# Kernel tuning notes

Hardware: AMD Instinct MI355X
Metric: run time of the kernel (lower is better)

## Reference

```python
import jax, jax.numpy as jnp
import numpy as np

B, S, E = 2, 2048, 2048
HQ, HKV, D = 16, 4, 128
WINDOW = 512
ROPE_BASE = 10000.0


def apply_rope(x):
    # x: [B, H, S, D]; rotate-half RoPE, positions start at 0 (prefill, no cache)
    half = x.shape[-1] // 2
    inv_freq = 1.0 / (ROPE_BASE ** (jnp.arange(half, dtype=jnp.float32) / half))
    ang = jnp.arange(x.shape[2], dtype=jnp.float32)[:, None] * inv_freq[None, :]  # [S, half]
    cos, sin = jnp.cos(ang), jnp.sin(ang)
    x1, x2 = x[..., :half], x[..., half:]
    return jnp.concatenate([x1 * cos - x2 * sin, x1 * sin + x2 * cos], axis=-1)


def setup_inputs() -> dict:
    key = jax.random.key(0)
    ks = jax.random.split(key, 9)
    sc = 0.02
    return {
        "x": jax.random.normal(ks[0], (B, S, E), dtype=jnp.float32),
        "Wq": jax.random.normal(ks[1], (HQ * D, E), dtype=jnp.float32) * sc,
        "bq": jnp.zeros((HQ * D,), dtype=jnp.float32),
        "Wk": jax.random.normal(ks[2], (HKV * D, E), dtype=jnp.float32) * sc,
        "bk": jnp.zeros((HKV * D,), dtype=jnp.float32),
        "Wv": jax.random.normal(ks[3], (HKV * D, E), dtype=jnp.float32) * sc,
        "bv": jnp.zeros((HKV * D,), dtype=jnp.float32),
        "Wo": jax.random.normal(ks[4], (E, HQ * D), dtype=jnp.float32) * sc,
        "bo": jnp.zeros((E,), dtype=jnp.float32),
    }


def reference(x, Wq, bq, Wk, bk, Wv, bv, Wo, bo):
    b, s, _ = x.shape
    group = HQ // HKV
    # projections (torch Linear: y = x @ W.T + b)
    Q = (x @ Wq.T + bq).reshape(b, s, HQ, D).transpose(0, 2, 1, 3)     # [B,HQ,S,D]
    K = (x @ Wk.T + bk).reshape(b, s, HKV, D).transpose(0, 2, 1, 3)    # [B,HKV,S,D]
    V = (x @ Wv.T + bv).reshape(b, s, HKV, D).transpose(0, 2, 1, 3)
    Q = apply_rope(Q)
    K = apply_rope(K)
    # GQA: group query heads per KV head instead of repeating K/V (same math)
    Qg = Q.reshape(b, HKV, group, s, D)
    scores = jnp.einsum('bkgqd,bkyd->bkgqy', Qg, K) / jnp.sqrt(jnp.float32(D))
    # sliding-window causal mask: j <= i and i - j <= window_size
    i = jnp.arange(s)[:, None]
    j = jnp.arange(s)[None, :]
    allowed = (j <= i) & ((i - j) <= WINDOW)
    scores = jnp.where(allowed, scores, jnp.float32(-jnp.inf))
    w = jax.nn.softmax(scores, axis=-1)
    out = jnp.einsum('bkgqy,bkyd->bkgqd', w, V)                        # [B,HKV,G,S,D]
    out = out.reshape(b, HQ, s, D).transpose(0, 2, 1, 3).reshape(b, s, HQ * D)
    out = out @ Wo.T + bo  # dropout is identity at inference
    return out
```

## Files before the change

### kernel.cpp

```cpp
#include <hip/hip_runtime.h>
#include <hip/hip_bf16.h>

typedef unsigned short u16;
typedef unsigned int u32;
typedef __attribute__((ext_vector_type(4))) unsigned short ushort4_t;
typedef __attribute__((ext_vector_type(8))) short short8;
typedef __attribute__((ext_vector_type(4))) float f32x4;

#define B_ 2
#define S_ 2048
#define E_ 2048
#define HQ_ 16
#define HKV_ 4
#define D_ 128
#define WINDOW_ 512

static __device__ __forceinline__ float bf2f(u16 u) {
    union { unsigned int i; float f; } v; v.i = ((unsigned int)u) << 16; return v.f;
}
static __device__ __forceinline__ u16 f2bf(float f) {
    unsigned int x = __float_as_uint(f);
    unsigned int r = (x + 0x7fffu + ((x >> 16) & 1u)) >> 16;
    return (u16)r;
}

static __device__ __forceinline__ void gload_lds16(const u16* g, u16* l) {
    __builtin_amdgcn_global_load_lds(
        (const __attribute__((address_space(1))) unsigned int*)g,
        (__attribute__((address_space(3))) unsigned int*)l,
        16, 0, 0);
}

static __device__ __forceinline__ int detect_fp32(const u16* wq, int* cnt_sh) {
    if (threadIdx.x == 0) *cnt_sh = 0;
    __syncthreads();
    int c = 0;
    #pragma unroll
    for (int k = 0; k < 4; ++k) {
        u16 v = wq[threadIdx.x * 4 + k];
        if (((v >> 7) & 0xFF) >= 0x90) c++;
    }
    atomicAdd(cnt_sh, c);
    __syncthreads();
    return (*cnt_sh >= 64) ? 1 : 0;
}

#define C_WQ   8388608u
#define C_WK   12582912u
#define C_WV   13631488u
#define C_BQ   14680064u
#define C_BK   14682112u
#define C_BV   14682624u
#define C_WO   14683136u
#define C_BO   18877440u
#define NTOT   18879488u

__global__ __launch_bounds__(256) void convert_kernel(
    const void* p0, const void* p1, const void* p2, const void* p3, const void* p4,
    const void* p5, const void* p6, const void* p7, const void* p8,
    u16* __restrict__ C, int* __restrict__ flagout)
{
    __shared__ int cnt;
    const int f = detect_fp32((const u16*)p1, &cnt);
    if (blockIdx.x == 0 && threadIdx.x == 0) *flagout = f;

    unsigned int idx = (blockIdx.x * 256u + threadIdx.x) * 4u;
    if (idx >= NTOT) return;

    const void* src; unsigned int local;
    if      (idx < C_WQ) { src = p0; local = idx; }
    else if (idx < C_WK) { src = p1; local = idx - C_WQ; }
    else if (idx < C_WV) { src = p3; local = idx - C_WK; }
    else if (idx < C_BQ) { src = p5; local = idx - C_WV; }
    else if (idx < C_BK) { src = p2; local = idx - C_BQ; }
    else if (idx < C_BV) { src = p4; local = idx - C_BK; }
    else if (idx < C_WO) { src = p6; local = idx - C_BV; }
    else if (idx < C_BO) { src = p7; local = idx - C_WO; }
    else                 { src = p8; local = idx - C_BO; }

    ushort4_t o;
    if (f) {
        float4 v = *(const float4*)((const float*)src + local);
        o[0] = f2bf(v.x); o[1] = f2bf(v.y); o[2] = f2bf(v.z); o[3] = f2bf(v.w);
    } else {
        o = *(const ushort4_t*)((const u16*)src + local);
    }
    *(ushort4_t*)(C + idx) = o;
}

__global__ __launch_bounds__(512, 2) void gemm256(
    const u16* __restrict__ A, const u16* __restrict__ W,
    const u16* __restrict__ bias, u16* __restrict__ C,
    int M, int N, int K)
{
    __shared__ __align__(16) u16 lds[65536];

    const int m0 = blockIdx.y * 256, n0 = blockIdx.x * 256;
    const int t = threadIdx.x;
    const int wv = t >> 6, lane = t & 63;
    const int wm = wv >> 2, wn = wv & 3;
    const int quad = lane >> 4, l16 = lane & 15;
    const int h3 = l16 & 7;

    const int rr = t >> 3;
    const int sblk = ((t & 7) ^ (rr & 7)) * 8;

    const u16* Asrc = A + (size_t)(m0 + rr) * K + sblk;
    const u16* Bsrc = W + (size_t)(n0 + rr) * K + sblk;
    u16* ldsA = lds + wv * 512;
    u16* ldsB = lds + 16384 + wv * 512;

#define STAGE_A(slot, Qi, k0) gload_lds16(Asrc + (size_t)((Qi) * 64) * K + (k0), ldsA + (slot) * 32768 + (Qi) * 4096)
#define STAGE_B(slot, Qi, k0) gload_lds16(Bsrc + (size_t)((Qi) * 64) * K + (k0), ldsB + (slot) * 32768 + (Qi) * 4096)

    f32x4 acc[8][4];
    #pragma unroll
    for (int mi = 0; mi < 8; ++mi)
        #pragma unroll
        for (int ni = 0; ni < 4; ++ni)
            acc[mi][ni] = (f32x4){0.f, 0.f, 0.f, 0.f};

    const int NT = K / 64;

    #pragma unroll
    for (int q = 0; q < 4; ++q) STAGE_A(0, q, 0);
    #pragma unroll
    for (int q = 0; q < 4; ++q) STAGE_B(0, q, 0);
    __builtin_amdgcn_sched_barrier(0);
    #pragma unroll
    for (int q = 0; q < 4; ++q) STAGE_A(1, q, 64);
    #pragma unroll
    for (int q = 0; q < 4; ++q) STAGE_B(1, q, 64);
    __builtin_amdgcn_sched_barrier(0);

    short8 afr[4][2];
    short8 b0[2][2], b1[2][2];

#define DSREAD_A(qm_)                                                          \
    _Pragma("unroll")                                                          \
    for (int f = 0; f < 4; ++f) {                                              \
        const int r = wm * 128 + (qm_) * 64 + f * 16 + l16;                    \
        _Pragma("unroll")                                                      \
        for (int kk = 0; kk < 2; ++kk)                                         \
            afr[f][kk] = *(const short8*)(As + r * 64 + (((kk * 4 + quad) ^ h3) << 3)); \
    }

#define DSREAD_B(dst, qn_)                                                     \
    _Pragma("unroll")                                                          \
    for (int g = 0; g < 2; ++g) {                                              \
        const int r = wn * 64 + (qn_) * 32 + g * 16 + l16;                     \
        _Pragma("unroll")                                                      \
        for (int kk = 0; kk < 2; ++kk)                                         \
            dst[g][kk] = *(const short8*)(Bs + r * 64 + (((kk * 4 + quad) ^ h3) << 3)); \
    }

#define SYNC_MFMA(qm_, bsel, qn_)                                              \
    __builtin_amdgcn_sched_barrier(0);                                         \
    __builtin_amdgcn_s_barrier();                                              \
    asm volatile("s_waitcnt lgkmcnt(0)" ::: "memory");                         \
    __builtin_amdgcn_sched_barrier(0);                                         \
    __builtin_amdgcn_s_setprio(1);                                             \
    _Pragma("unroll")                                                          \
    for (int g = 0; g < 2; ++g)                                                \
        _Pragma("unroll")                                                      \
        for (int f = 0; f < 4; ++f)                                            \
            _Pragma("unroll")                                                  \
            for (int kk = 0; kk < 2; ++kk)                                     \
                acc[(qm_) * 4 + f][(qn_) * 2 + g] =                            \
                    __builtin_amdgcn_mfma_f32_16x16x32_bf16(                   \
                        afr[f][kk], bsel[g][kk], acc[(qm_) * 4 + f][(qn_) * 2 + g], 0, 0, 0); \
    __builtin_amdgcn_s_setprio(0);                                             \
    __builtin_amdgcn_sched_barrier(0);                                         \
    __builtin_amdgcn_s_barrier();                                              \
    __builtin_amdgcn_sched_barrier(0);

    for (int kt = 0; kt < NT; ++kt) {
        const int slot = kt & 1;
        const u16* As = lds + slot * 32768;
        const u16* Bs = As + 16384;

        if (kt == 0)           asm volatile("s_waitcnt vmcnt(8)" ::: "memory");
        else if (kt == NT - 1) asm volatile("s_waitcnt vmcnt(0)" ::: "memory");
        else                   asm volatile("s_waitcnt vmcnt(2)" ::: "memory");
        __builtin_amdgcn_s_barrier();
        __builtin_amdgcn_sched_barrier(0);

        const int kB = (kt + 1) * 64;
        const int kA = (kt + 2) * 64;
        const int sB = slot ^ 1;
        const bool doB = (kt >= 1) && (kt <= NT - 2);
        const bool doA = (kt <= NT - 3);

        DSREAD_A(0);
        DSREAD_B(b0, 0);
        if (doB) { STAGE_A(sB, 1, kB); STAGE_A(sB, 3, kB);
                   STAGE_B(sB, 0, kB); STAGE_B(sB, 1, kB); }
        SYNC_MFMA(0, b0, 0);

        DSREAD_B(b1, 1);
        if (doB) { STAGE_B(sB, 2, kB); STAGE_B(sB, 3, kB); }
        SYNC_MFMA(0, b1, 1);

        DSREAD_A(1);
        if (doA) { STAGE_A(slot, 0, kA); }
        SYNC_MFMA(1, b1, 1);

        if (doA) { STAGE_A(slot, 2, kA); }
        SYNC_MFMA(1, b0, 0);
    }

#undef STAGE_A
#undef STAGE_B
#undef DSREAD_A
#undef DSREAD_B
#undef SYNC_MFMA

    #pragma unroll
    for (int mi = 0; mi < 8; ++mi) {
        #pragma unroll
        for (int ni = 0; ni < 4; ++ni) {
            const int row0 = m0 + wm * 128 + mi * 16 + quad * 4;
            const int col  = n0 + wn * 64 + ni * 16 + l16;
            const float bb = bf2f(bias[col]);
            #pragma unroll
            for (int r = 0; r < 4; ++r)
                C[(size_t)(row0 + r) * N + col] = f2bf(acc[mi][ni][r] + bb);
        }
    }
}

#define TBK 32

__global__ __launch_bounds__(256) void gemm128_out(
    const u16* __restrict__ A, const u16* __restrict__ W,
    const u16* __restrict__ bias, void* __restrict__ Cout,
    int M, int N, int K, const int* __restrict__ flagp)
{
    __shared__ __align__(16) u16 As[128 * TBK];
    __shared__ __align__(16) u16 Bs[128 * TBK];

    const int m0 = blockIdx.y * 128, n0 = blockIdx.x * 128;

    const int t = threadIdx.x;
    const int wv = t >> 6, lane = t & 63;
    const int waveM = wv >> 1, waveN = wv & 1;
    const int quad = lane >> 4, l16 = lane & 15;

    const int lrow = lane >> 2;
    const int lcol = (lane & 3) * 8;

    f32x4 acc[4][4];
    #pragma unroll
    for (int mi = 0; mi < 4; ++mi)
        #pragma unroll
        for (int ni = 0; ni < 4; ++ni)
            acc[mi][ni] = (f32x4){0.f, 0.f, 0.f, 0.f};

    const u16* ga = A + (size_t)(m0 + wv * 32 + lrow) * K + lcol;
    const u16* gb = W + (size_t)(n0 + wv * 32 + lrow) * K + lcol;
    u16* la0 = As + (wv * 32) * TBK;
    u16* la1 = As + (wv * 32 + 16) * TBK;
    u16* lb0 = Bs + (wv * 32) * TBK;
    u16* lb1 = Bs + (wv * 32 + 16) * TBK;

    for (int k0 = 0; k0 < K; k0 += TBK) {
        __syncthreads();
        gload_lds16(ga + k0, la0);
        gload_lds16(ga + k0 + (size_t)16 * K, la1);
        gload_lds16(gb + k0, lb0);
        gload_lds16(gb + k0 + (size_t)16 * K, lb1);
        __syncthreads();

        short8 af[4];
        #pragma unroll
        for (int mi = 0; mi < 4; ++mi)
            af[mi] = *(const short8*)(As + (waveM * 64 + mi * 16 + l16) * TBK + quad * 8);
        #pragma unroll
        for (int ni = 0; ni < 4; ++ni) {
            short8 bf = *(const short8*)(Bs + (waveN * 64 + ni * 16 + l16) * TBK + quad * 8);
            #pragma unroll
            for (int mi = 0; mi < 4; ++mi)
                acc[mi][ni] = __builtin_amdgcn_mfma_f32_16x16x32_bf16(af[mi], bf, acc[mi][ni], 0, 0, 0);
        }
    }

    const int f = *flagp;
    #pragma unroll
    for (int mi = 0; mi < 4; ++mi) {
        #pragma unroll
        for (int ni = 0; ni < 4; ++ni) {
            int row0 = m0 + waveM * 64 + mi * 16 + quad * 4;
            int col  = n0 + waveN * 64 + ni * 16 + l16;
            float bb = bf2f(bias[col]);
            #pragma unroll
            for (int r = 0; r < 4; ++r) {
                float val = acc[mi][ni][r] + bb;
                size_t idx = (size_t)(row0 + r) * N + col;
                if (f) ((float*)Cout)[idx] = val;
                else   ((u16*)Cout)[idx]   = f2bf(val);
            }
        }
    }
}

#define ROPE_BLOCKS 20480

__global__ __launch_bounds__(256) void rope_transpose(
    u16* __restrict__ QKV, u16* __restrict__ VT)
{
    if (blockIdx.x < ROPE_BLOCKS) {
        const size_t qtot = (size_t)B_ * S_ * HQ_ * 64;
        size_t idx = (size_t)blockIdx.x * 256 + threadIdx.x;

        int d; size_t tok; u16* p;
        if (idx < qtot) {
            d = (int)(idx & 63);
            size_t th = idx >> 6;
            int h = (int)(th & 15);
            tok = th >> 4;
            p = QKV + tok * 3072 + h * 128 + d;
        } else {
            size_t r = idx - qtot;
            d = (int)(r & 63);
            size_t th = r >> 6;
            int kh = (int)(th & 3);
            tok = th >> 2;
            p = QKV + tok * 3072 + 2048 + kh * 128 + d;
        }
        int s = (int)(tok & (S_ - 1));

        float x1 = bf2f(p[0]);
        float x2 = bf2f(p[64]);
        float inv_freq = __expf(-0.14391156514f * (float)d);
        float ang = (float)s * inv_freq;
        float sn, cs;
        __sincosf(ang, &sn, &cs);
        p[0]  = f2bf(x1 * cs - x2 * sn);
        p[64] = f2bf(x1 * sn + x2 * cs);
    } else {
        const int bid = blockIdx.x - ROPE_BLOCKS;
        const int t = threadIdx.x;
        const int s_blk = bid & 63;
        const int dh = (bid >> 6) & 1;
        const int bkh = bid >> 7;
        const int b = bkh >> 2, kh = bkh & 3;

        const int d = dh * 64 + (t & 63);
        const int s0 = s_blk * 32 + (t >> 6) * 8;

        const u16* src = QKV + (size_t)(b * S_ + s0) * 3072 + 2560 + kh * 128 + d;
        short8 v;
        #pragma unroll
        for (int j = 0; j < 8; ++j)
            v[j] = (short)src[(size_t)j * 3072];
        *(short8*)(VT + ((size_t)(bkh * 128 + d)) * S_ + s0) = v;
    }
}

__global__ __launch_bounds__(256) void attn_mfma(
    const u16* __restrict__ QKV, const u16* __restrict__ VT, u16* __restrict__ O)
{
    __shared__ __align__(16) u16 Ks[32 * 136];
    __shared__ __align__(16) u16 Vs[128 * 40];
    __shared__ __align__(16) u16 ps[4][16 * 40];

    const int t = threadIdx.x;
    const int wv = t >> 6, lane = t & 63;
    const int quad = lane >> 4, l16 = lane & 15;

    const int h = blockIdx.x & 15;
    const int tile = (blockIdx.x >> 4) & 31;
    const int b = blockIdx.x >> 9;
    const int kh = h >> 2;

    const int i0b = tile * 64;
    const int i0w = i0b + wv * 16;
    const float scale = 0.08838834764831845f;
    const float CEXP = 8.0f;

    short8 qf[4];
    {
        const u16* qrow = QKV + (size_t)(b * S_ + i0w + l16) * 3072 + h * 128 + quad * 8;
        #pragma unroll
        for (int kc = 0; kc < 4; ++kc)
            qf[kc] = *(const short8*)(qrow + kc * 32);
    }

    short8 ones;
    #pragma unroll
    for (int j = 0; j < 8; ++j) ones[j] = (short)0x3F80;

    f32x4 oc[8];
    #pragma unroll
    for (int c = 0; c < 8; ++c) oc[c] = (f32x4){0.f, 0.f, 0.f, 0.f};
    f32x4 ocl = (f32x4){0.f, 0.f, 0.f, 0.f};

    int jlo = i0b - WINDOW_; if (jlo < 0) jlo = 0;
    const int nblk = (i0b + 64 - jlo) >> 5;

    const u16* VTb = VT + (size_t)(b * 4 + kh) * 128 * S_;

    for (int blk = 0; blk < nblk; ++blk) {
        const int jbase = jlo + blk * 32;
        __syncthreads();
        #pragma unroll
        for (int it = 0; it < 2; ++it) {
            int idx = it * 256 + t;
            int key = idx >> 4;
            int c8  = (idx & 15) * 8;
            int row = ((key & 1) << 4) | (key >> 1);
            short8 kvv = *(const short8*)(QKV + (size_t)(b * S_ + jbase + key) * 3072 + 2048 + kh * 128 + c8);
            *(short8*)(Ks + row * 136 + c8) = kvv;
        }
        #pragma unroll
        for (int it = 0; it < 2; ++it) {
            int idx = it * 256 + t;
            int d = idx >> 2;
            int q4 = idx & 3;
            short8 vvv = *(const short8*)(VTb + (size_t)d * S_ + jbase + q4 * 8);
            *(short8*)(Vs + d * 40 + q4 * 8) = vvv;
        }
        __syncthreads();

        bool active = (jbase <= i0w + 15) && (jbase + 31 >= i0w - WINDOW_);
        if (!active) continue;

        f32x4 sc0 = {0.f,0.f,0.f,0.f}, sc1 = {0.f,0.f,0.f,0.f};
        #pragma unroll
        for (int kc = 0; kc < 4; ++kc) {
            short8 kb0 = *(const short8*)(Ks + l16 * 136 + kc * 32 + quad * 8);
            short8 kb1 = *(const short8*)(Ks + (16 + l16) * 136 + kc * 32 + quad * 8);
            sc0 = __builtin_amdgcn_mfma_f32_16x16x32_bf16(qf[kc], kb0, sc0, 0, 0, 0);
            sc1 = __builtin_amdgcn_mfma_f32_16x16x32_bf16(qf[kc], kb1, sc1, 0, 0, 0);
        }

        const int j0 = jbase + 2 * l16;
        const int iq = i0w + quad * 4;
        u16* pw = ps[wv];
        #pragma unroll
        for (int r = 0; r < 4; ++r) {
            int i = iq + r;
            bool ok0 = (unsigned)(i - j0)     <= (unsigned)WINDOW_;
            bool ok1 = (unsigned)(i - j0 - 1) <= (unsigned)WINDOW_;
            float p0 = ok0 ? __expf(sc0[r] * scale - CEXP) : 0.f;
            float p1 = ok1 ? __expf(sc1[r] * scale - CEXP) : 0.f;
            u32 pk = ((u32)f2bf(p1) << 16) | (u32)f2bf(p0);
            *(u32*)(pw + (quad * 4 + r) * 40 + 2 * l16) = pk;
        }
        short8 pa = *(const short8*)(pw + l16 * 40 + quad * 8);

        #pragma unroll
        for (int c = 0; c < 8; ++c) {
            short8 vb = *(const short8*)(Vs + (c * 16 + l16) * 40 + quad * 8);
            oc[c] = __builtin_amdgcn_mfma_f32_16x16x32_bf16(pa, vb, oc[c], 0, 0, 0);
        }
        ocl = __builtin_amdgcn_mfma_f32_16x16x32_bf16(pa, ones, ocl, 0, 0, 0);
    }

    float inv0[4];
    #pragma unroll
    for (int r = 0; r < 4; ++r) inv0[r] = 1.0f / ocl[r];
    #pragma unroll
    for (int c = 0; c < 8; ++c) {
        #pragma unroll
        for (int r = 0; r < 4; ++r) {
            O[((size_t)(b * S_ + i0w + quad * 4 + r) * HQ_ + h) * D_ + c * 16 + l16] =
                f2bf(oc[c][r] * inv0[r]);
        }
    }
}

extern "C" void kernel_launch(void* const* d_in, const int* in_sizes, int n_in,
                              void* d_out, int out_size, void* d_ws, size_t ws_size,
                              hipStream_t stream)
{
    char* ws = (char*)d_ws;
    u16* Cc   = (u16*)ws;
    int* flag = (int*)(ws + 37758976);
    u16* QKV  = (u16*)(ws + 37759232);
    u16* Ab   = (u16*)(ws + 37759232 + 25165824);

    const u16* xb    = Cc;
    u16*       VT    = Cc;
    const u16* Wqkv  = Cc + C_WQ;
    const u16* bqkv  = Cc + C_BQ;
    const u16* Wob   = Cc + C_WO;
    const u16* bob   = Cc + C_BO;

    const int M = B_ * S_;
    dim3 blk(256);

    convert_kernel<<<dim3(NTOT / 4 / 256), blk, 0, stream>>>(
        d_in[0], d_in[1], d_in[2], d_in[3], d_in[4], d_in[5], d_in[6], d_in[7], d_in[8],
        Cc, flag);

    gemm256<<<dim3(3072 / 256, M / 256), dim3(512), 0, stream>>>(
        xb, Wqkv, bqkv, QKV, M, 3072, E_);

    rope_transpose<<<dim3(ROPE_BLOCKS + 1024), blk, 0, stream>>>(QKV, VT);

    attn_mfma<<<dim3(B_ * HQ_ * (S_ / 64)), blk, 0, stream>>>(QKV, VT, Ab);

    gemm128_out<<<dim3(E_ / 128, M / 128), blk, 0, stream>>>(Ab, Wob, bob, d_out, M, E_, HQ_ * D_, flag);
}
```

Before: 317.4 us.

## Restructure GEMM main loop to one mid-iteration barrier with double A fragments

Rewrites the software pipeline of the projection GEMM inner loop. Both A-fragment halves are now loaded into separate register sets up front, and fine-grained lgkmcnt waits let MFMAs start while later LDS reads are still in flight. The four barrier-bracketed MFMA phases become a single mid-iteration barrier, and the prologue/staging schedule is reshuffled so all B and odd-A quarters are issued together. This cuts synchronisation stalls per k-step at the cost of extra VGPRs for the second A fragment set, which may affect occupancy, and depends on the hand-counted waitcnt values being correct.

Result: no change. 313.6 us (-1.2%).

```diff
diff --git a/kernel.cpp b/kernel.cpp
--- a/kernel.cpp
+++ b/kernel.cpp
@@ -127,22 +127,20 @@
     #pragma unroll
     for (int q = 0; q < 4; ++q) STAGE_B(0, q, 0);
     __builtin_amdgcn_sched_barrier(0);
-    #pragma unroll
-    for (int q = 0; q < 4; ++q) STAGE_A(1, q, 64);
-    #pragma unroll
-    for (int q = 0; q < 4; ++q) STAGE_B(1, q, 64);
+    STAGE_A(1, 0, 64);
+    STAGE_A(1, 2, 64);
     __builtin_amdgcn_sched_barrier(0);
 
-    short8 afr[4][2];
+    short8 aA[4][2], aB[4][2];
     short8 b0[2][2], b1[2][2];
 
-#define DSREAD_A(qm_)                                                          \
+#define DSREAD_A(dst, qm_)                                                     \
     _Pragma("unroll")                                                          \
-    for (int f = 0; f < 4; ++f) {                                              \
-        const int r = wm * 128 + (qm_) * 64 + f * 16 + l16;                    \
+    for (int fr = 0; fr < 4; ++fr) {                                           \
+        const int r = wm * 128 + (qm_) * 64 + fr * 16 + l16;                   \
         _Pragma("unroll")                                                      \
         for (int kk = 0; kk < 2; ++kk)                                         \
-            afr[f][kk] = *(const short8*)(As + r * 64 + (((kk * 4 + quad) ^ h3) << 3)); \
+            dst[fr][kk] = *(const short8*)(As + r * 64 + (((kk * 4 + quad) ^ h3) << 3)); \
     }
 
 #define DSREAD_B(dst, qn_)                                                     \
@@ -154,66 +152,76 @@
             dst[g][kk] = *(const short8*)(Bs + r * 64 + (((kk * 4 + quad) ^ h3) << 3)); \
     }
 
-#define SYNC_MFMA(qm_, bsel, qn_)                                              \
-    __builtin_amdgcn_sched_barrier(0);                                         \
-    __builtin_amdgcn_s_barrier();                                              \
-    asm volatile("s_waitcnt lgkmcnt(0)" ::: "memory");                         \
-    __builtin_amdgcn_sched_barrier(0);                                         \
+#define MFMA_PH(qm_, afrag, bfrag, qn_)                                        \
     __builtin_amdgcn_s_setprio(1);                                             \
     _Pragma("unroll")                                                          \
     for (int g = 0; g < 2; ++g)                                                \
         _Pragma("unroll")                                                      \
-        for (int f = 0; f < 4; ++f)                                            \
+        for (int fr = 0; fr < 4; ++fr)                                         \
             _Pragma("unroll")                                                  \
             for (int kk = 0; kk < 2; ++kk)                                     \
-                acc[(qm_) * 4 + f][(qn_) * 2 + g] =                            \
+                acc[(qm_) * 4 + fr][(qn_) * 2 + g] =                           \
                     __builtin_amdgcn_mfma_f32_16x16x32_bf16(                   \
-                        afr[f][kk], bsel[g][kk], acc[(qm_) * 4 + f][(qn_) * 2 + g], 0, 0, 0); \
-    __builtin_amdgcn_s_setprio(0);                                             \
-    __builtin_amdgcn_sched_barrier(0);                                         \
-    __builtin_amdgcn_s_barrier();                                              \
-    __builtin_amdgcn_sched_barrier(0);
+                        afrag[fr][kk], bfrag[g][kk], acc[(qm_) * 4 + fr][(qn_) * 2 + g], 0, 0, 0); \
+    __builtin_amdgcn_s_setprio(0);
 
     for (int kt = 0; kt < NT; ++kt) {
         const int slot = kt & 1;
         const u16* As = lds + slot * 32768;
         const u16* Bs = As + 16384;
 
-        if (kt == 0)           asm volatile("s_waitcnt vmcnt(8)" ::: "memory");
-        else if (kt == NT - 1) asm volatile("s_waitcnt vmcnt(0)" ::: "memory");
-        else                   asm volatile("s_waitcnt vmcnt(2)" ::: "memory");
+        if (kt == NT - 1) asm volatile("s_waitcnt vmcnt(0)" ::: "memory");
+        else              asm volatile("s_waitcnt vmcnt(2)" ::: "memory");
         __builtin_amdgcn_s_barrier();
         __builtin_amdgcn_sched_barrier(0);
 
         const int kB = (kt + 1) * 64;
         const int kA = (kt + 2) * 64;
         const int sB = slot ^ 1;
-        const bool doB = (kt >= 1) && (kt <= NT - 2);
-        const bool doA = (kt <= NT - 3);
-
-        DSREAD_A(0);
+        const bool doEarly = (kt <= NT - 2);
+        const bool doMid   = (kt <= NT - 3);
+
+        DSREAD_A(aA, 0);
         DSREAD_B(b0, 0);
-        if (doB) { STAGE_A(sB, 1, kB); STAGE_A(sB, 3, kB);
-                   STAGE_B(sB, 0, kB); STAGE_B(sB, 1, kB); }
-        SYNC_MFMA(0, b0, 0);
-
+        __builtin_amdgcn_sched_barrier(0);
         DSREAD_B(b1, 1);
-        if (doB) { STAGE_B(sB, 2, kB); STAGE_B(sB, 3, kB); }
-        SYNC_MFMA(0, b1, 1);
-
-        DSREAD_A(1);
-        if (doA) { STAGE_A(slot, 0, kA); }
-        SYNC_MFMA(1, b1, 1);
-
-        if (doA) { STAGE_A(slot, 2, kA); }
-        SYNC_MFMA(1, b0, 0);
+        __builtin_amdgcn_sched_barrier(0);
+
+        if (doEarly) { STAGE_A(sB, 1, kB); STAGE_A(sB, 3, kB);
+                       STAGE_B(sB, 0, kB); STAGE_B(sB, 1, kB);
+                       STAGE_B(sB, 2, kB); STAGE_B(sB, 3, kB); }
+        __builtin_amdgcn_sched_barrier(0);
+
+        asm volatile("s_waitcnt lgkmcnt(4)" ::: "memory");
+        __builtin_amdgcn_sched_barrier(0);
+        DSREAD_A(aB, 1);
+        __builtin_amdgcn_sched_barrier(0);
+
+        MFMA_PH(0, aA, b0, 0);
+        __builtin_amdgcn_sched_barrier(0);
+        asm volatile("s_waitcnt lgkmcnt(8)" ::: "memory");
+        __builtin_amdgcn_sched_barrier(0);
+        MFMA_PH(0, aA, b1, 1);
+        __builtin_amdgcn_sched_barrier(0);
+        asm volatile("s_waitcnt lgkmcnt(0)" ::: "memory");
+        __builtin_amdgcn_sched_barrier(0);
+        __builtin_amdgcn_s_barrier();
+        __builtin_amdgcn_sched_barrier(0);
+
+        if (doMid) { STAGE_A(slot, 0, kA); STAGE_A(slot, 2, kA); }
+        __builtin_amdgcn_sched_barrier(0);
+
+        MFMA_PH(1, aB, b1, 1);
+        __builtin_amdgcn_sched_barrier(0);
+        MFMA_PH(1, aB, b0, 0);
+        __builtin_amdgcn_sched_barrier(0);
     }
 
 #undef STAGE_A
 #undef STAGE_B
 #undef DSREAD_A
 #undef DSREAD_B
-#undef SYNC_MFMA
+#undef MFMA_PH
 
     #pragma unroll
     for (int mi = 0; mi < 8; ++mi) {
```
